# Kernel optimization log

Hardware: AMD Instinct MI355X
Metric: run time of the kernel (lower is better)

Reference implementation:

```python
import jax, jax.numpy as jnp
import numpy as np

B, L, D = 2, 2048, 2048
N, K, H = 16, 8, 128
EPS = 1e-6
ROPE_THETA = 1000000
K_MASK = -2.3819763e+38


def rms_norm(x, w, eps=EPS):
    dtype = x.dtype
    rms = jnp.sqrt(jnp.mean(x.astype(jnp.float32) ** 2, axis=-1, keepdims=True) + eps)
    return (w * x / rms).astype(dtype)


def apply_rope(inputs, positions, head_dim, rope_theta=ROPE_THETA):
    # inputs: [B, L, n, H], positions: [B, L]
    fraction = 2 * jnp.arange(0, head_dim // 2, dtype=jnp.float32) / head_dim
    timescale = rope_theta ** fraction  # [H/2]
    sinusoid = positions[..., jnp.newaxis] / timescale[jnp.newaxis, jnp.newaxis, :]  # [B,L,H/2]
    sinusoid = sinusoid[..., jnp.newaxis, :]  # [B,L,1,H/2]
    sin, cos = jnp.sin(sinusoid), jnp.cos(sinusoid)
    first, second = jnp.split(inputs, 2, axis=-1)
    out = jnp.concatenate([first * cos - second * sin, second * cos + first * sin], axis=-1)
    return out.astype(inputs.dtype)


def setup_inputs() -> dict:
    key = jax.random.key(0)
    ks = jax.random.split(key, 6)
    x = jax.random.normal(ks[0], (B, L, D), dtype=jnp.float32)
    position_ids = jnp.broadcast_to(jnp.arange(L, dtype=jnp.int32)[None, :], (B, L))
    # causal mask [B, L, S]
    attn_mask = jnp.broadcast_to(jnp.tril(jnp.ones((L, L), dtype=bool))[None], (B, L, L))
    wq = jax.random.normal(ks[1], (D, N, H), dtype=jnp.float32) * 0.02
    wk = jax.random.normal(ks[2], (D, K, H), dtype=jnp.float32) * 0.02
    wv = jax.random.normal(ks[3], (D, K, H), dtype=jnp.float32) * 0.02
    wo = jax.random.normal(ks[4], (N, H, D), dtype=jnp.float32) * 0.02
    q_norm_w = jnp.ones((H,), dtype=jnp.float32)
    k_norm_w = jnp.ones((H,), dtype=jnp.float32)
    return {"x": x, "position_ids": position_ids, "attn_mask": attn_mask,
            "wq": wq, "wk": wk, "wv": wv, "wo": wo,
            "q_norm_w": q_norm_w, "k_norm_w": k_norm_w}


def reference(x, position_ids, attn_mask, wq, wk, wv, wo, q_norm_w, k_norm_w):
    scale = H ** (-0.5)
    q = jnp.einsum('BLD,DNH->BLNH', x, wq)  # [B,L,N,H]
    k = jnp.einsum('BSD,DKH->BSKH', x, wk)  # [B,S,K,H]
    v = jnp.einsum('BSD,DKH->BSKH', x, wv)
    q = rms_norm(q, q_norm_w)
    k = rms_norm(k, k_norm_w)
    q = apply_rope(q, position_ids, H)
    k = apply_rope(k, position_ids, H)
    b, l, n, h = q.shape
    s = k.shape[1]
    kk = k.shape[2]
    q = q.reshape((b, l, kk, n // kk, h))
    attn = jnp.einsum('BLKGH,BSKH->BKGLS', q, k) * scale
    attn = attn.reshape((b, n, l, s))
    attn = jnp.where(jnp.expand_dims(attn_mask, -3), attn, K_MASK)
    attn = jax.nn.softmax(attn.astype(jnp.float32), axis=-1).astype(k.dtype)
    attn = attn.reshape((b, kk, n // kk, l, s))
    qkv = jnp.einsum('BKGLS,BSKH->BLKGH', attn, v).reshape((b, l, n, h))
    out = jnp.einsum('BLNH,NHD->BLD', qkv, wo)
    return out
```

## Files before the change

### kernel.cpp

```cpp
#include <hip/hip_runtime.h>

#define B_ 2
#define L_ 2048
#define D_ 2048
#define NH_ 16
#define KH_ 8
#define HD_ 128

typedef __attribute__((ext_vector_type(8))) short short8;
typedef __attribute__((ext_vector_type(4))) float floatx4;

__device__ __forceinline__ unsigned short f2bf(float f) {
  unsigned u = __float_as_uint(f);
  unsigned r = (u + 0x7fffu + ((u >> 16) & 1u)) >> 16;
  return (unsigned short)r;
}
__device__ __forceinline__ float bf2f(unsigned short h) {
  return __uint_as_float(((unsigned)h) << 16);
}
__device__ __forceinline__ void gl_lds16(const void* g, void* l) {
  __builtin_amdgcn_global_load_lds(
      (const __attribute__((address_space(1))) unsigned int*)g,
      (__attribute__((address_space(3))) unsigned int*)l, 16, 0, 0);
}

__global__ __launch_bounds__(256) void cvt_f32_bf16(const float* __restrict__ in,
                                                    unsigned short* __restrict__ out) {
  long i = ((long)blockIdx.x * 256 + threadIdx.x) * 4;
  float4 v = *(const float4*)(in + i);
  ushort4 o;
  o.x = f2bf(v.x); o.y = f2bf(v.y); o.z = f2bf(v.z); o.w = f2bf(v.w);
  *(ushort4*)(out + i) = o;
}

__global__ __launch_bounds__(256) void transpose_cvt(const float* __restrict__ in,
                                                     unsigned short* __restrict__ out,
                                                     int R, int C, int ostride) {
  __shared__ float tile[32][33];
  int c0 = blockIdx.x * 32, r0 = blockIdx.y * 32;
  int tx = threadIdx.x, ty = threadIdx.y;
#pragma unroll
  for (int i = 0; i < 4; i++)
    tile[ty + i * 8][tx] = in[(long)(r0 + ty + i * 8) * C + c0 + tx];
  __syncthreads();
#pragma unroll
  for (int i = 0; i < 4; i++) {
    int oc = ty + i * 8;
    out[(long)(c0 + oc) * ostride + r0 + tx] = f2bf(tile[tx][oc]);
  }
}

__global__ __launch_bounds__(256) void transpose_v(const unsigned short* __restrict__ qkv,
                                                   unsigned short* __restrict__ vT) {
  __shared__ unsigned short tile[32][33];
  int l0 = blockIdx.x * 32, h0 = blockIdx.y * 32;
  int bk = blockIdx.z;
  int b = bk >> 3, kh = bk & 7;
  int tx = threadIdx.x, ty = threadIdx.y;
  const unsigned short* src = qkv + (long)b * L_ * 4096 + 3072 + kh * 128;
#pragma unroll
  for (int i = 0; i < 4; i++)
    tile[ty + i * 8][tx] = src[(long)(l0 + ty + i * 8) * 4096 + h0 + tx];
  __syncthreads();
  unsigned short* dst = vT + (long)bk * HD_ * L_;
#pragma unroll
  for (int i = 0; i < 4; i++)
    dst[(long)(h0 + ty + i * 8) * L_ + l0 + tx] = tile[tx][ty + i * 8];
}

template <int OUT_BF16>
__global__ __launch_bounds__(256, 2) void gemm128(const unsigned short* __restrict__ A,
                                                  const unsigned short* __restrict__ Bt,
                                                  void* __restrict__ C,
                                                  int M, int N, int K) {
  __shared__ unsigned short As[128 * 64];
  __shared__ unsigned short Bs[128 * 64];
  const int t = threadIdx.x;
  const int lane = t & 63, w = t >> 6;
  const int wy = w >> 1, wx = w & 1;
  const int col = lane & 15, quad = lane >> 4;
  const long m0 = (long)blockIdx.y * 128, n0 = (long)blockIdx.x * 128;
  floatx4 acc[4][4];
#pragma unroll
  for (int i = 0; i < 4; i++)
#pragma unroll
    for (int j = 0; j < 4; j++) acc[i][j] = (floatx4)0.0f;
  const int rs = t >> 3, bs = t & 7;
  for (int kt = 0; kt < K; kt += 64) {
#pragma unroll
    for (int i = 0; i < 4; i++) {
      int r = i * 32 + rs;
      gl_lds16(A + (m0 + r) * (long)K + kt + ((bs ^ (r & 7)) << 3),
               &As[(i * 32 + w * 8) * 64]);
      gl_lds16(Bt + (n0 + r) * (long)K + kt + ((bs ^ (r & 7)) << 3),
               &Bs[(i * 32 + w * 8) * 64]);
    }
    __syncthreads();
#pragma unroll
    for (int ks = 0; ks < 2; ks++) {
      short8 af[4], bf[4];
#pragma unroll
      for (int mi = 0; mi < 4; mi++) {
        int row = wy * 64 + mi * 16 + col;
        int blk = ks * 4 + quad;
        af[mi] = *(const short8*)&As[row * 64 + ((blk ^ (row & 7)) << 3)];
      }
#pragma unroll
      for (int ni = 0; ni < 4; ni++) {
        int row = wx * 64 + ni * 16 + col;
        int blk = ks * 4 + quad;
        bf[ni] = *(const short8*)&Bs[row * 64 + ((blk ^ (row & 7)) << 3)];
      }
#pragma unroll
      for (int mi = 0; mi < 4; mi++)
#pragma unroll
        for (int ni = 0; ni < 4; ni++)
          acc[mi][ni] = __builtin_amdgcn_mfma_f32_16x16x32_bf16(af[mi], bf[ni],
                                                                acc[mi][ni], 0, 0, 0);
    }
    __syncthreads();
  }
#pragma unroll
  for (int mi = 0; mi < 4; mi++)
#pragma unroll
    for (int r = 0; r < 4; r++) {
      long row = m0 + wy * 64 + mi * 16 + quad * 4 + r;
#pragma unroll
      for (int ni = 0; ni < 4; ni++) {
        long cg = n0 + wx * 64 + ni * 16 + col;
        float val = acc[mi][ni][r];
        if (OUT_BF16)
          ((unsigned short*)C)[row * N + cg] = f2bf(val);
        else
          ((float*)C)[row * N + cg] = val;
      }
    }
}

__global__ __launch_bounds__(256) void rmsrope(const unsigned short* __restrict__ qkv,
                                               const int* __restrict__ pos,
                                               const float* __restrict__ qw,
                                               const float* __restrict__ kw,
                                               unsigned short* __restrict__ qo,
                                               unsigned short* __restrict__ ko) {
  const int t = threadIdx.x, lane = t & 63, w = t >> 6;
  const int gid = blockIdx.x * 4 + w;
  const int row = gid / 24;
  const int hd = gid - row * 24;
  const int b = row >> 11, l = row & 2047;
  const unsigned short* src = qkv + (long)row * 4096 + hd * 128;
  float x0 = bf2f(src[lane]);
  float x1 = bf2f(src[lane + 64]);
  float ss = x0 * x0 + x1 * x1;
#pragma unroll
  for (int off = 32; off; off >>= 1) ss += __shfl_xor(ss, off);
  float inv = 1.0f / sqrtf(ss * (1.0f / 128.0f) + 1e-6f);
  const float* nw = (hd < 16) ? qw : kw;
  x0 = nw[lane] * x0 * inv;
  x1 = nw[lane + 64] * x1 * inv;
  float p = (float)pos[row];
  float ts = powf(1.0e6f, (float)lane * (1.0f / 64.0f));
  float ang = p / ts;
  float s, c;
  sincosf(ang, &s, &c);
  float o0 = x0 * c - x1 * s;
  float o1 = x1 * c + x0 * s;
  unsigned short* dst;
  if (hd < 16) {
    const float QSC = 0.08838834764831845f * 1.4426950408889634f;
    o0 *= QSC;
    o1 *= QSC;
    dst = qo + (((long)b * NH_ + hd) * L_ + l) * HD_;
  } else {
    dst = ko + (((long)b * KH_ + (hd - 16)) * L_ + l) * HD_;
  }
  dst[lane] = f2bf(o0);
  dst[lane + 64] = f2bf(o1);
}

__global__ __launch_bounds__(256, 2) void flash(const unsigned short* __restrict__ Q,
                                                const unsigned short* __restrict__ Kg,
                                                const unsigned short* __restrict__ VT,
                                                unsigned short* __restrict__ Og) {
  __shared__ unsigned short Ks[64 * 128];
  __shared__ unsigned short Vs[128 * 64];
  __shared__ unsigned short Ps[128 * 72];
  const int n = blockIdx.y, b = blockIdx.z;
  const int qt = b ? (15 - blockIdx.x) : blockIdx.x;
  const int t = threadIdx.x, lane = t & 63, w = t >> 6;
  const int col = lane & 15, quad = lane >> 4;
  const int kvh = n >> 1;
  const unsigned short* kb = Kg + ((long)b * KH_ + kvh) * L_ * HD_;
  const unsigned short* vtb = VT + ((long)b * KH_ + kvh) * HD_ * L_;
  const int l0 = qt * 128;
  const int steps = 2 * qt + 2;
  const unsigned short* qb = Q + (((long)b * NH_ + n) * L_ + l0) * HD_;

  short8 qf[2][4];
#pragma unroll
  for (int mi = 0; mi < 2; mi++)
#pragma unroll
    for (int ks = 0; ks < 4; ks++)
      qf[mi][ks] = *(const short8*)(qb + (w * 32 + mi * 16 + col) * 128 + ks * 32 + quad * 8);

  floatx4 o[2][8];
#pragma unroll
  for (int mi = 0; mi < 2; mi++)
#pragma unroll
    for (int nf = 0; nf < 8; nf++) o[mi][nf] = (floatx4)0.0f;
  float lrow[2][4];
#pragma unroll
  for (int mi = 0; mi < 2; mi++)
#pragma unroll
    for (int r = 0; r < 4; r++) lrow[mi][r] = 0.0f;

  for (int st = 0; st < steps; st++) {
    const int s0 = st * 64;
    {
      const int rK = t >> 4, blkK = t & 15;
#pragma unroll
      for (int i = 0; i < 4; i++) {
        int r = i * 16 + rK;
        int gblk = (blkK & 8) | ((blkK ^ r) & 7);
        gl_lds16(kb + (long)(s0 + r) * 128 + gblk * 8, &Ks[(i * 16 + w * 4) * 128]);
      }
    }
    {
      const int rV = t >> 3, blkV = t & 7;
#pragma unroll
      for (int j = 0; j < 4; j++) {
        int r = j * 32 + rV;
        int gblk = (blkV ^ r) & 7;
        gl_lds16(vtb + (long)r * L_ + s0 + gblk * 8, &Vs[(j * 32 + w * 8) * 64]);
      }
    }
    __syncthreads();

    floatx4 sa[2][4];
#pragma unroll
    for (int mi = 0; mi < 2; mi++)
#pragma unroll
      for (int sf = 0; sf < 4; sf++) sa[mi][sf] = (floatx4)0.0f;
#pragma unroll
    for (int ks = 0; ks < 4; ks++) {
      short8 bf[4];
#pragma unroll
      for (int sf = 0; sf < 4; sf++) {
        int srow = sf * 16 + col;
        int blk = ks * 4 + quad;
        bf[sf] = *(const short8*)&Ks[srow * 128 + (((blk & 8) | ((blk ^ srow) & 7)) << 3)];
      }
#pragma unroll
      for (int mi = 0; mi < 2; mi++)
#pragma unroll
        for (int sf = 0; sf < 4; sf++)
          sa[mi][sf] = __builtin_amdgcn_mfma_f32_16x16x32_bf16(qf[mi][ks], bf[sf],
                                                               sa[mi][sf], 0, 0, 0);
    }

    if (st >= steps - 2) {
#pragma unroll
      for (int mi = 0; mi < 2; mi++)
#pragma unroll
        for (int sf = 0; sf < 4; sf++)
#pragma unroll
          for (int r = 0; r < 4; r++) {
            int lr = l0 + w * 32 + mi * 16 + quad * 4 + r;
            int sr = s0 + sf * 16 + col;
            if (sr > lr) sa[mi][sf][r] = -3.0e38f;
          }
    }

#pragma unroll
    for (int mi = 0; mi < 2; mi++)
#pragma unroll
      for (int sf = 0; sf < 4; sf++)
#pragma unroll
        for (int r = 0; r < 4; r++) {
          float pv = exp2f(sa[mi][sf][r] - 17.0f);
          sa[mi][sf][r] = pv;
          lrow[mi][r] += pv;
        }

#pragma unroll
    for (int mi = 0; mi < 2; mi++)
#pragma unroll
      for (int sf = 0; sf < 4; sf++)
#pragma unroll
        for (int r = 0; r < 4; r++)
          Ps[(w * 32 + mi * 16 + quad * 4 + r) * 72 + sf * 16 + col] = f2bf(sa[mi][sf][r]);

#pragma unroll
    for (int ks = 0; ks < 2; ks++) {
      short8 pf[2];
#pragma unroll
      for (int mi = 0; mi < 2; mi++)
        pf[mi] = *(const short8*)&Ps[(w * 32 + mi * 16 + col) * 72 + ks * 32 + quad * 8];
      short8 vf[8];
#pragma unroll
      for (int nf = 0; nf < 8; nf++) {
        int h = nf * 16 + col;
        int blk = ks * 4 + quad;
        vf[nf] = *(const short8*)&Vs[h * 64 + ((blk ^ (h & 7)) << 3)];
      }
#pragma unroll
      for (int mi = 0; mi < 2; mi++)
#pragma unroll
        for (int nf = 0; nf < 8; nf++)
          o[mi][nf] = __builtin_amdgcn_mfma_f32_16x16x32_bf16(pf[mi], vf[nf],
                                                              o[mi][nf], 0, 0, 0);
    }
    __syncthreads();
  }

#pragma unroll
  for (int mi = 0; mi < 2; mi++)
#pragma unroll
    for (int r = 0; r < 4; r++) {
      float s = lrow[mi][r];
#pragma unroll
      for (int off = 8; off; off >>= 1) s += __shfl_xor(s, off);
      float inv = 1.0f / s;
      int lg = l0 + w * 32 + mi * 16 + quad * 4 + r;
      unsigned short* dst = Og + (((long)b * L_ + lg) * NH_ + n) * HD_;
#pragma unroll
      for (int nf = 0; nf < 8; nf++)
        dst[nf * 16 + col] = f2bf(o[mi][nf][r] * inv);
    }
}

extern "C" void kernel_launch(void* const* d_in, const int* in_sizes, int n_in,
                              void* d_out, int out_size, void* d_ws, size_t ws_size,
                              hipStream_t stream) {
  const float* x = (const float*)d_in[0];
  const int* pos = (const int*)d_in[1];
  const float* wq = (const float*)d_in[3];
  const float* wk = (const float*)d_in[4];
  const float* wv = (const float*)d_in[5];
  const float* wo = (const float*)d_in[6];
  const float* qnw = (const float*)d_in[7];
  const float* knw = (const float*)d_in[8];
  float* out = (float*)d_out;

  char* ws = (char*)d_ws;
  unsigned short* xb     = (unsigned short*)(ws + 0);
  unsigned short* wqkv_t = (unsigned short*)(ws + 16777216);
  unsigned short* wo_t   = (unsigned short*)(ws + 33554432);
  unsigned short* qkv    = (unsigned short*)(ws + 41943040);
  unsigned short* q      = (unsigned short*)(ws + 75497472);
  unsigned short* k      = (unsigned short*)(ws + 92274688);
  unsigned short* vT     = (unsigned short*)(ws + 100663296);
  unsigned short* ao     = (unsigned short*)(ws + 109051904);
  if (ws_size < 125829120) return;

  cvt_f32_bf16<<<8192, 256, 0, stream>>>(x, xb);
  dim3 tb(32, 8);
  transpose_cvt<<<dim3(64, 64), tb, 0, stream>>>(wq, wqkv_t, 2048, 2048, 2048);
  transpose_cvt<<<dim3(32, 64), tb, 0, stream>>>(wk, wqkv_t + 2048L * 2048, 2048, 1024, 2048);
  transpose_cvt<<<dim3(32, 64), tb, 0, stream>>>(wv, wqkv_t + 3072L * 2048, 2048, 1024, 2048);
  transpose_cvt<<<dim3(64, 64), tb, 0, stream>>>(wo, wo_t, 2048, 2048, 2048);
  gemm128<1><<<dim3(32, 32), 256, 0, stream>>>(xb, wqkv_t, qkv, 4096, 4096, 2048);
  rmsrope<<<24576, 256, 0, stream>>>(qkv, pos, qnw, knw, q, k);
  transpose_v<<<dim3(64, 4, 16), tb, 0, stream>>>(qkv, vT);
  flash<<<dim3(16, NH_, B_), 256, 0, stream>>>(q, k, vT, ao);
  gemm128<0><<<dim3(16, 32), 256, 0, stream>>>(ao, wo_t, out, 4096, 2048, 2048);
}
```

Baseline: 393.5 us.

## Split flash KV range across blocks with combine pass and split-K output GEMM

The flash attention grid doubles: each block pairs a short and a long causal query tile and processes alternating KV steps, writing unnormalised partial outputs and row sums. A new combine kernel merges the two halves and normalises them. The output projection uses split-K over two z-slices with atomic adds into a zeroed output. Launch bounds rise to 4 blocks per CU, the P tile reuses the K shared buffer with an XOR swizzle, and the RoPE powf is replaced by exp2f. The goal is better occupancy and load balance, at the cost of extra memory traffic for partials, a memset and atomics.

Result: slower. 728.6 us (+85.2%).

```diff
diff --git a/kernel.cpp b/kernel.cpp
--- a/kernel.cpp
+++ b/kernel.cpp
@@ -68,8 +68,8 @@
     dst[(long)(h0 + ty + i * 8) * L_ + l0 + tx] = tile[tx][ty + i * 8];
 }
 
-template <int OUT_BF16>
-__global__ __launch_bounds__(256, 2) void gemm128(const unsigned short* __restrict__ A,
+template <int MODE>
+__global__ __launch_bounds__(256, 4) void gemm128(const unsigned short* __restrict__ A,
                                                   const unsigned short* __restrict__ Bt,
                                                   void* __restrict__ C,
                                                   int M, int N, int K) {
@@ -80,13 +80,15 @@
   const int wy = w >> 1, wx = w & 1;
   const int col = lane & 15, quad = lane >> 4;
   const long m0 = (long)blockIdx.y * 128, n0 = (long)blockIdx.x * 128;
+  const int kbeg = (MODE == 2) ? blockIdx.z * (K >> 1) : 0;
+  const int kend = (MODE == 2) ? kbeg + (K >> 1) : K;
   floatx4 acc[4][4];
 #pragma unroll
   for (int i = 0; i < 4; i++)
 #pragma unroll
     for (int j = 0; j < 4; j++) acc[i][j] = (floatx4)0.0f;
   const int rs = t >> 3, bs = t & 7;
-  for (int kt = 0; kt < K; kt += 64) {
+  for (int kt = kbeg; kt < kend; kt += 64) {
 #pragma unroll
     for (int i = 0; i < 4; i++) {
       int r = i * 32 + rs;
@@ -129,10 +131,12 @@
       for (int ni = 0; ni < 4; ni++) {
         long cg = n0 + wx * 64 + ni * 16 + col;
         float val = acc[mi][ni][r];
-        if (OUT_BF16)
+        if (MODE == 1)
           ((unsigned short*)C)[row * N + cg] = f2bf(val);
+        else if (MODE == 0)
+          ((float*)C)[row * N + cg] = val;
         else
-          ((float*)C)[row * N + cg] = val;
+          unsafeAtomicAdd(&((float*)C)[row * N + cg], val);
       }
     }
 }
@@ -159,8 +163,7 @@
   x0 = nw[lane] * x0 * inv;
   x1 = nw[lane + 64] * x1 * inv;
   float p = (float)pos[row];
-  float ts = powf(1.0e6f, (float)lane * (1.0f / 64.0f));
-  float ang = p / ts;
+  float ang = p * exp2f((float)lane * -0.31143075889f);
   float s, c;
   sincosf(ang, &s, &c);
   float o0 = x0 * c - x1 * s;
@@ -178,155 +181,181 @@
   dst[lane + 64] = f2bf(o1);
 }
 
-__global__ __launch_bounds__(256, 2) void flash(const unsigned short* __restrict__ Q,
+__global__ __launch_bounds__(256, 4) void flash(const unsigned short* __restrict__ Q,
                                                 const unsigned short* __restrict__ Kg,
                                                 const unsigned short* __restrict__ VT,
-                                                unsigned short* __restrict__ Og) {
+                                                unsigned short* __restrict__ O0,
+                                                unsigned short* __restrict__ O1,
+                                                float* __restrict__ ls0,
+                                                float* __restrict__ ls1) {
   __shared__ unsigned short Ks[64 * 128];
   __shared__ unsigned short Vs[128 * 64];
-  __shared__ unsigned short Ps[128 * 72];
+  unsigned short* Ps = Ks;
   const int n = blockIdx.y, b = blockIdx.z;
-  const int qt = b ? (15 - blockIdx.x) : blockIdx.x;
+  const int ip = blockIdx.x >> 1, hp = blockIdx.x & 1;
   const int t = threadIdx.x, lane = t & 63, w = t >> 6;
   const int col = lane & 15, quad = lane >> 4;
   const int kvh = n >> 1;
   const unsigned short* kb = Kg + ((long)b * KH_ + kvh) * L_ * HD_;
   const unsigned short* vtb = VT + ((long)b * KH_ + kvh) * HD_ * L_;
-  const int l0 = qt * 128;
-  const int steps = 2 * qt + 2;
-  const unsigned short* qb = Q + (((long)b * NH_ + n) * L_ + l0) * HD_;
-
-  short8 qf[2][4];
-#pragma unroll
-  for (int mi = 0; mi < 2; mi++)
-#pragma unroll
-    for (int ks = 0; ks < 4; ks++)
-      qf[mi][ks] = *(const short8*)(qb + (w * 32 + mi * 16 + col) * 128 + ks * 32 + quad * 8);
-
-  floatx4 o[2][8];
-#pragma unroll
-  for (int mi = 0; mi < 2; mi++)
-#pragma unroll
-    for (int nf = 0; nf < 8; nf++) o[mi][nf] = (floatx4)0.0f;
-  float lrow[2][4];
-#pragma unroll
-  for (int mi = 0; mi < 2; mi++)
-#pragma unroll
-    for (int r = 0; r < 4; r++) lrow[mi][r] = 0.0f;
-
-  for (int st = 0; st < steps; st++) {
-    const int s0 = st * 64;
-    {
-      const int rK = t >> 4, blkK = t & 15;
-#pragma unroll
-      for (int i = 0; i < 4; i++) {
-        int r = i * 16 + rK;
-        int gblk = (blkK & 8) | ((blkK ^ r) & 7);
-        gl_lds16(kb + (long)(s0 + r) * 128 + gblk * 8, &Ks[(i * 16 + w * 4) * 128]);
-      }
+  const long bn = (long)b * NH_ + n;
+
+  for (int phase = 0; phase < 2; phase++) {
+    const int qt = phase ? (15 - ip) : ip;
+    const int half = phase ? (1 - hp) : hp;
+    const int l0 = qt * 128;
+    const unsigned short* qb = Q + (bn * L_ + l0) * HD_;
+    unsigned short* Ow = half ? O1 : O0;
+    float* lsw = half ? ls1 : ls0;
+
+    short8 qf[2][4];
+#pragma unroll
+    for (int mi = 0; mi < 2; mi++)
+#pragma unroll
+      for (int ks = 0; ks < 4; ks++)
+        qf[mi][ks] = *(const short8*)(qb + (w * 32 + mi * 16 + col) * 128 + ks * 32 + quad * 8);
+
+    floatx4 o[2][8];
+#pragma unroll
+    for (int mi = 0; mi < 2; mi++)
+#pragma unroll
+      for (int nf = 0; nf < 8; nf++) o[mi][nf] = (floatx4)0.0f;
+    float lrow[2][4];
+#pragma unroll
+    for (int mi = 0; mi < 2; mi++)
+#pragma unroll
+      for (int r = 0; r < 4; r++) lrow[mi][r] = 0.0f;
+
+    for (int st = half; st < 2 * qt + 2; st += 2) {
+      const int s0 = st * 64;
+      {
+        const int rK = t >> 4, blkK = t & 15;
+#pragma unroll
+        for (int i = 0; i < 4; i++) {
+          int r = i * 16 + rK;
+          int gblk = (blkK & 8) | ((blkK ^ r) & 7);
+          gl_lds16(kb + (long)(s0 + r) * 128 + gblk * 8, &Ks[(i * 16 + w * 4) * 128]);
+        }
+      }
+      {
+        const int rV = t >> 3, blkV = t & 7;
+#pragma unroll
+        for (int j = 0; j < 4; j++) {
+          int r = j * 32 + rV;
+          int gblk = (blkV ^ r) & 7;
+          gl_lds16(vtb + (long)r * L_ + s0 + gblk * 8, &Vs[(j * 32 + w * 8) * 64]);
+        }
+      }
+      __syncthreads();
+
+      floatx4 sa[2][4];
+#pragma unroll
+      for (int mi = 0; mi < 2; mi++)
+#pragma unroll
+        for (int sf = 0; sf < 4; sf++) sa[mi][sf] = (floatx4)0.0f;
+#pragma unroll
+      for (int ks = 0; ks < 4; ks++) {
+        short8 bf[4];
+#pragma unroll
+        for (int sf = 0; sf < 4; sf++) {
+          int srow = sf * 16 + col;
+          int blk = ks * 4 + quad;
+          bf[sf] = *(const short8*)&Ks[srow * 128 + (((blk & 8) | ((blk ^ srow) & 7)) << 3)];
+        }
+#pragma unroll
+        for (int mi = 0; mi < 2; mi++)
+#pragma unroll
+          for (int sf = 0; sf < 4; sf++)
+            sa[mi][sf] = __builtin_amdgcn_mfma_f32_16x16x32_bf16(qf[mi][ks], bf[sf],
+                                                                 sa[mi][sf], 0, 0, 0);
+      }
+      __syncthreads();
+
+      if (st >= 2 * qt) {
+#pragma unroll
+        for (int mi = 0; mi < 2; mi++)
+#pragma unroll
+          for (int sf = 0; sf < 4; sf++)
+#pragma unroll
+            for (int r = 0; r < 4; r++) {
+              int lr = l0 + w * 32 + mi * 16 + quad * 4 + r;
+              int sr = s0 + sf * 16 + col;
+              if (sr > lr) sa[mi][sf][r] = -3.0e38f;
+            }
+      }
+
+#pragma unroll
+      for (int mi = 0; mi < 2; mi++)
+#pragma unroll
+        for (int sf = 0; sf < 4; sf++)
+#pragma unroll
+          for (int r = 0; r < 4; r++) {
+            float pv = exp2f(sa[mi][sf][r] - 17.0f);
+            lrow[mi][r] += pv;
+            int prow = w * 32 + mi * 16 + quad * 4 + r;
+            int scol = sf * 16 + col;
+            Ps[prow * 64 + (((scol >> 3) ^ (prow & 7)) << 3) + (scol & 7)] = f2bf(pv);
+          }
+
+#pragma unroll
+      for (int ks = 0; ks < 2; ks++) {
+        short8 pf[2];
+#pragma unroll
+        for (int mi = 0; mi < 2; mi++) {
+          int prow = w * 32 + mi * 16 + col;
+          int blk = ks * 4 + quad;
+          pf[mi] = *(const short8*)&Ps[prow * 64 + ((blk ^ (prow & 7)) << 3)];
+        }
+        short8 vf[8];
+#pragma unroll
+        for (int nf = 0; nf < 8; nf++) {
+          int h = nf * 16 + col;
+          int blk = ks * 4 + quad;
+          vf[nf] = *(const short8*)&Vs[h * 64 + ((blk ^ (h & 7)) << 3)];
+        }
+#pragma unroll
+        for (int mi = 0; mi < 2; mi++)
+#pragma unroll
+          for (int nf = 0; nf < 8; nf++)
+            o[mi][nf] = __builtin_amdgcn_mfma_f32_16x16x32_bf16(pf[mi], vf[nf],
+                                                                o[mi][nf], 0, 0, 0);
+      }
+      __syncthreads();
     }
-    {
-      const int rV = t >> 3, blkV = t & 7;
-#pragma unroll
-      for (int j = 0; j < 4; j++) {
-        int r = j * 32 + rV;
-        int gblk = (blkV ^ r) & 7;
-        gl_lds16(vtb + (long)r * L_ + s0 + gblk * 8, &Vs[(j * 32 + w * 8) * 64]);
-      }
-    }
-    __syncthreads();
-
-    floatx4 sa[2][4];
+
 #pragma unroll
     for (int mi = 0; mi < 2; mi++)
 #pragma unroll
-      for (int sf = 0; sf < 4; sf++) sa[mi][sf] = (floatx4)0.0f;
-#pragma unroll
-    for (int ks = 0; ks < 4; ks++) {
-      short8 bf[4];
-#pragma unroll
-      for (int sf = 0; sf < 4; sf++) {
-        int srow = sf * 16 + col;
-        int blk = ks * 4 + quad;
-        bf[sf] = *(const short8*)&Ks[srow * 128 + (((blk & 8) | ((blk ^ srow) & 7)) << 3)];
-      }
-#pragma unroll
-      for (int mi = 0; mi < 2; mi++)
-#pragma unroll
-        for (int sf = 0; sf < 4; sf++)
-          sa[mi][sf] = __builtin_amdgcn_mfma_f32_16x16x32_bf16(qf[mi][ks], bf[sf],
-                                                               sa[mi][sf], 0, 0, 0);
-    }
-
-    if (st >= steps - 2) {
-#pragma unroll
-      for (int mi = 0; mi < 2; mi++)
-#pragma unroll
-        for (int sf = 0; sf < 4; sf++)
-#pragma unroll
-          for (int r = 0; r < 4; r++) {
-            int lr = l0 + w * 32 + mi * 16 + quad * 4 + r;
-            int sr = s0 + sf * 16 + col;
-            if (sr > lr) sa[mi][sf][r] = -3.0e38f;
-          }
-    }
-
-#pragma unroll
-    for (int mi = 0; mi < 2; mi++)
-#pragma unroll
-      for (int sf = 0; sf < 4; sf++)
-#pragma unroll
-        for (int r = 0; r < 4; r++) {
-          float pv = exp2f(sa[mi][sf][r] - 17.0f);
-          sa[mi][sf][r] = pv;
-          lrow[mi][r] += pv;
-        }
-
-#pragma unroll
-    for (int mi = 0; mi < 2; mi++)
-#pragma unroll
-      for (int sf = 0; sf < 4; sf++)
-#pragma unroll
-        for (int r = 0; r < 4; r++)
-          Ps[(w * 32 + mi * 16 + quad * 4 + r) * 72 + sf * 16 + col] = f2bf(sa[mi][sf][r]);
-
-#pragma unroll
-    for (int ks = 0; ks < 2; ks++) {
-      short8 pf[2];
-#pragma unroll
-      for (int mi = 0; mi < 2; mi++)
-        pf[mi] = *(const short8*)&Ps[(w * 32 + mi * 16 + col) * 72 + ks * 32 + quad * 8];
-      short8 vf[8];
-#pragma unroll
-      for (int nf = 0; nf < 8; nf++) {
-        int h = nf * 16 + col;
-        int blk = ks * 4 + quad;
-        vf[nf] = *(const short8*)&Vs[h * 64 + ((blk ^ (h & 7)) << 3)];
-      }
-#pragma unroll
-      for (int mi = 0; mi < 2; mi++)
+      for (int r = 0; r < 4; r++) {
+        float s = lrow[mi][r];
+#pragma unroll
+        for (int off = 8; off; off >>= 1) s += __shfl_xor(s, off);
+        int lg = l0 + w * 32 + mi * 16 + quad * 4 + r;
+        if (col == 0) lsw[bn * L_ + lg] = s;
+        unsigned short* dst = Ow + (bn * L_ + lg) * HD_;
 #pragma unroll
         for (int nf = 0; nf < 8; nf++)
-          o[mi][nf] = __builtin_amdgcn_mfma_f32_16x16x32_bf16(pf[mi], vf[nf],
-                                                              o[mi][nf], 0, 0, 0);
-    }
-    __syncthreads();
+          dst[nf * 16 + col] = f2bf(o[mi][nf][r]);
+      }
   }
-
-#pragma unroll
-  for (int mi = 0; mi < 2; mi++)
-#pragma unroll
-    for (int r = 0; r < 4; r++) {
-      float s = lrow[mi][r];
-#pragma unroll
-      for (int off = 8; off; off >>= 1) s += __shfl_xor(s, off);
-      float inv = 1.0f / s;
-      int lg = l0 + w * 32 + mi * 16 + quad * 4 + r;
-      unsigned short* dst = Og + (((long)b * L_ + lg) * NH_ + n) * HD_;
-#pragma unroll
-      for (int nf = 0; nf < 8; nf++)
-        dst[nf * 16 + col] = f2bf(o[mi][nf][r] * inv);
-    }
+}
+
+__global__ __launch_bounds__(256) void combine(const unsigned short* __restrict__ O0,
+                                               const unsigned short* __restrict__ O1,
+                                               const float* __restrict__ ls0,
+                                               const float* __restrict__ ls1,
+                                               unsigned short* __restrict__ ao) {
+  int wid = blockIdx.x * 4 + (threadIdx.x >> 6);
+  int lane = threadIdx.x & 63;
+  int b = wid >> 15, rem = wid & 32767, n = rem >> 11, l = rem & 2047;
+  long off = (long)wid * 128 + lane * 2;
+  float inv = 1.0f / (ls0[wid] + ls1[wid]);
+  ushort2 a = *(const ushort2*)(O0 + off);
+  ushort2 c = *(const ushort2*)(O1 + off);
+  ushort2 o;
+  o.x = f2bf((bf2f(a.x) + bf2f(c.x)) * inv);
+  o.y = f2bf((bf2f(a.y) + bf2f(c.y)) * inv);
+  *(ushort2*)(ao + (((long)(b * 2048 + l) * 16 + n) * 128 + lane * 2)) = o;
 }
 
 extern "C" void kernel_launch(void* const* d_in, const int* in_sizes, int n_in,
@@ -351,8 +380,13 @@
   unsigned short* k      = (unsigned short*)(ws + 92274688);
   unsigned short* vT     = (unsigned short*)(ws + 100663296);
   unsigned short* ao     = (unsigned short*)(ws + 109051904);
+  unsigned short* Op0    = (unsigned short*)(ws + 0);
+  unsigned short* Op1    = (unsigned short*)(ws + 16777216);
+  float* ls0             = (float*)(ws + 41943040);
+  float* ls1             = (float*)(ws + 42205184);
   if (ws_size < 125829120) return;
 
+  hipMemsetAsync(d_out, 0, (size_t)out_size * 4, stream);
   cvt_f32_bf16<<<8192, 256, 0, stream>>>(x, xb);
   dim3 tb(32, 8);
   transpose_cvt<<<dim3(64, 64), tb, 0, stream>>>(wq, wqkv_t, 2048, 2048, 2048);
@@ -362,6 +396,7 @@
   gemm128<1><<<dim3(32, 32), 256, 0, stream>>>(xb, wqkv_t, qkv, 4096, 4096, 2048);
   rmsrope<<<24576, 256, 0, stream>>>(qkv, pos, qnw, knw, q, k);
   transpose_v<<<dim3(64, 4, 16), tb, 0, stream>>>(qkv, vT);
-  flash<<<dim3(16, NH_, B_), 256, 0, stream>>>(q, k, vT, ao);
-  gemm128<0><<<dim3(16, 32), 256, 0, stream>>>(ao, wo_t, out, 4096, 2048, 2048);
-}
+  flash<<<dim3(32, NH_, B_), 256, 0, stream>>>(q, k, vT, Op0, Op1, ls0, ls1);
+  combine<<<16384, 256, 0, stream>>>(Op0, Op1, ls0, ls1, ao);
+  gemm128<2><<<dim3(16, 32, 2), 256, 0, stream>>>(ao, wo_t, out, 4096, 2048, 2048);
+}
```
